# Kernel tuning notes

Hardware: AMD Instinct MI355X
Metric: run time of the kernel (lower is better)

Reference implementation:

```python
import jax, jax.numpy as jnp
import numpy as np

HIDDEN = 768
INTER = 1536
N_EXPERTS = 8
TOP_K = 2
AUX_COEF = 0.01


def setup_inputs() -> dict:
    key = jax.random.key(0)
    k0, k1, k2, k3, k4 = jax.random.split(key, 5)
    B, S = 2, 1024
    x = jax.random.normal(k0, (B, S, HIDDEN), dtype=jnp.float32)
    # nn.Linear weights (no bias); stored pre-transposed for einsum (in, out)
    router_w = jax.random.normal(k1, (HIDDEN, N_EXPERTS), dtype=jnp.float32) * 0.02
    w_gate = jax.random.normal(k2, (N_EXPERTS, HIDDEN, INTER), dtype=jnp.float32) * 0.02
    w_up = jax.random.normal(k3, (N_EXPERTS, HIDDEN, INTER), dtype=jnp.float32) * 0.02
    w_down = jax.random.normal(k4, (N_EXPERTS, INTER, HIDDEN), dtype=jnp.float32) * 0.02
    return {"x": x, "router_w": router_w, "w_gate": w_gate, "w_up": w_up, "w_down": w_down}


def reference(x, router_w, w_gate, w_up, w_down):
    B, S, H = x.shape
    xf = x.reshape(-1, H)                      # [T, H]
    T = xf.shape[0]

    router_logits = xf @ router_w              # [T, E]
    router_probs = jax.nn.softmax(router_logits.astype(jnp.float32), axis=-1)
    topk_probs, topk_idx = jax.lax.top_k(router_probs, TOP_K)   # [T, K]
    topk_probs = topk_probs / topk_probs.sum(axis=-1, keepdims=True)

    # dense combine weights: [T, E]; top_k indices are distinct per token so add == set
    comb = jnp.zeros((T, N_EXPERTS), jnp.float32).at[
        jnp.arange(T)[:, None], topk_idx
    ].add(topk_probs)

    # SwiGLU for all experts (dense faithful form of the per-expert gather loop)
    g = jnp.einsum("th,ehi->tei", xf, w_gate)  # [T, E, I]
    u = jnp.einsum("th,ehi->tei", xf, w_up)
    expert_out = jnp.einsum("tei,eih->teh", jax.nn.silu(g) * u, w_down)  # [T, E, H]
    out = jnp.einsum("teh,te->th", expert_out, comb.astype(expert_out.dtype))

    # load-balancing aux loss
    tokens_per_expert = jnp.zeros(N_EXPERTS, jnp.float32).at[topk_idx.reshape(-1)].add(1.0)
    tokens_per_expert = tokens_per_expert / (T * TOP_K)
    router_prob_per_expert = router_probs.mean(axis=0)
    aux_loss = N_EXPERTS * (tokens_per_expert * router_prob_per_expert).sum() * AUX_COEF

    return out.reshape(B, S, H), aux_loss
```

## Files before the change

kernel.cpp:

```cpp
#include <hip/hip_runtime.h>
#include <math.h>


typedef unsigned short u16;
typedef __attribute__((ext_vector_type(8))) short bhalf8;
typedef __attribute__((ext_vector_type(4))) float floatx4;

#define HD 768
#define ID 1536
#define NE 8
#define TT 2048
#define SLOTS 5120
#define MT 40
#define RBLK 512

__device__ __forceinline__ float b2f(u16 u) {
    union { unsigned int i; float f; } v; v.i = ((unsigned int)u) << 16; return v.f;
}
__device__ __forceinline__ u16 f2b(float f) {
    union { float f; unsigned int i; } v; v.f = f;
    unsigned int i = v.i;
    return (u16)((i + 0x7FFFu + ((i >> 16) & 1u)) >> 16);
}
__device__ __forceinline__ void glds16(const u16* g, u16* l) {
    __builtin_amdgcn_global_load_lds(
        (const __attribute__((address_space(1))) unsigned int*)g,
        (__attribute__((address_space(3))) unsigned int*)l, 16, 0, 0);
}

__global__ void init_k(const u16* __restrict__ x16, int* flag,
                       int* hdr, int* tokof, float* pslot) {
    int i = blockIdx.x * 256 + threadIdx.x;
    if (i < 40) hdr[i] = 0;
    if (i < SLOTS) { tokof[i] = -1; pslot[i] = 0.f; }
    if (blockIdx.x == 0 && threadIdx.x >= 64 && threadIdx.x < 128) {
        int lane = threadIdx.x - 64, c = 0;
#pragma unroll
        for (int j = 0; j < 4; ++j) {
            u16 w = x16[lane + 64 * j];
            int ex = (w >> 7) & 0xFF;
            c += (ex >= 118 && ex <= 135);
        }
#pragma unroll
        for (int off = 32; off > 0; off >>= 1) c += __shfl_xor(c, off);
        if (lane == 0) *flag = (c >= 200) ? 1 : 0;
    }
}

__global__ void router_k(const void* __restrict__ x, const void* __restrict__ rw,
                         const int* __restrict__ flag,
                         int* topki, float* topkp, float* blockpart) {
    __shared__ float sp[4][NE];
    int lane = threadIdx.x & 63, wave = threadIdx.x >> 6;
    int t = blockIdx.x * 4 + wave;
    int bf = *flag;
    const float* xf = (const float*)x + (size_t)t * HD;
    const u16*   xh = (const u16*)x + (size_t)t * HD;
    const float* rf = (const float*)rw;
    const u16*   rh = (const u16*)rw;
    float acc[NE];
#pragma unroll
    for (int e = 0; e < NE; ++e) acc[e] = 0.f;
    for (int j = 0; j < HD / 64; ++j) {
        int h = lane + 64 * j;
        float xv = bf ? b2f(xh[h]) : xf[h];
#pragma unroll
        for (int e = 0; e < NE; ++e)
            acc[e] += xv * (bf ? b2f(rh[h * NE + e]) : rf[h * NE + e]);
    }
#pragma unroll
    for (int e = 0; e < NE; ++e) {
        float v = acc[e];
#pragma unroll
        for (int off = 32; off > 0; off >>= 1) v += __shfl_xor(v, off);
        acc[e] = v;
    }
    if (lane == 0) {
        float m = acc[0];
        for (int e = 1; e < NE; ++e) m = fmaxf(m, acc[e]);
        float p[NE], s = 0.f;
        for (int e = 0; e < NE; ++e) { p[e] = expf(acc[e] - m); s += p[e]; }
        float inv = 1.f / s;
        for (int e = 0; e < NE; ++e) { p[e] *= inv; sp[wave][e] = p[e]; }
        int i1 = 0; float p1 = p[0];
        for (int e = 1; e < NE; ++e) if (p[e] > p1) { p1 = p[e]; i1 = e; }
        int i2 = -1; float p2 = -1.f;
        for (int e = 0; e < NE; ++e) if (e != i1 && p[e] > p2) { p2 = p[e]; i2 = e; }
        if (i2 < 0) { i2 = (i1 + 1) & 7; p2 = p[i2]; }
        float sn = 1.f / (p1 + p2);
        topki[2 * t] = i1;  topki[2 * t + 1] = i2;
        topkp[2 * t] = p1 * sn;  topkp[2 * t + 1] = p2 * sn;
    }
    __syncthreads();
    if (threadIdx.x < NE)
        blockpart[blockIdx.x * NE + threadIdx.x] =
            sp[0][threadIdx.x] + sp[1][threadIdx.x] +
            sp[2][threadIdx.x] + sp[3][threadIdx.x];
}

__global__ void prefix_k(const int* __restrict__ topki,
                         const float* __restrict__ blockpart, int* base,
                         int* total, int* cursor, void* out, const int* flag) {
    __shared__ int hist[NE];
    __shared__ float psum[NE];
    int tid = threadIdx.x;
    if (tid < NE) { hist[tid] = 0; psum[tid] = 0.f; }
    __syncthreads();
    for (int i = tid; i < TT * 2; i += 256) atomicAdd(&hist[topki[i] & 7], 1);
    for (int i = tid; i < RBLK * NE; i += 256) atomicAdd(&psum[i & 7], blockpart[i]);
    __syncthreads();
    if (tid == 0) {
        int cum = 0; float aux = 0.f;
        for (int e = 0; e < NE; ++e) {
            int c = hist[e];
            base[e] = cum; cum += (c + 127) & ~127;
            cursor[e] = 0;
            aux += ((float)c / (float)(TT * 2)) * (psum[e] / (float)TT);
        }
        *total = cum;
        float auxv = aux * (float)NE * 0.01f;
        if (*flag) ((u16*)out)[(size_t)TT * HD] = f2b(auxv);
        else       ((float*)out)[(size_t)TT * HD] = auxv;
    }
}

__global__ void scatter_k(const int* __restrict__ topki, const float* __restrict__ topkp,
                          const int* __restrict__ base, int* cursor,
                          int* tokof, float* pslot, int* slotmap) {
    __shared__ int lcnt[NE], lbase[NE];
    int tid = threadIdx.x;
    int t = blockIdx.x * 256 + tid;
    if (tid < NE) lcnt[tid] = 0;
    __syncthreads();
    int e0 = topki[2 * t] & 7, e1 = topki[2 * t + 1] & 7;
    float q0 = topkp[2 * t], q1 = topkp[2 * t + 1];
    int l0 = atomicAdd(&lcnt[e0], 1);
    int l1 = atomicAdd(&lcnt[e1], 1);
    __syncthreads();
    if (tid < NE) lbase[tid] = atomicAdd(&cursor[tid], lcnt[tid]);
    __syncthreads();
    int s0 = min(max(base[e0] + lbase[e0] + l0, 0), SLOTS - 1);
    int s1 = min(max(base[e1] + lbase[e1] + l1, 0), SLOTS - 1);
    tokof[s0] = t;  pslot[s0] = q0;  slotmap[2 * t] = s0;
    tokof[s1] = t;  pslot[s1] = q1;  slotmap[2 * t + 1] = s1;
}

__global__ void apack_k(const void* __restrict__ x, const int* __restrict__ flag,
                        const int* __restrict__ tokof, const int* __restrict__ total,
                        u16* __restrict__ apack) {
    int mt = blockIdx.y, kt = blockIdx.x;
    if (mt * 128 >= *total) return;
    int tid = threadIdx.x;
    int ml = tid >> 1, half = tid & 1;
    int tok = tokof[mt * 128 + ml];
    union { uint4 v[4]; u16 u[32]; } buf;
    if ((unsigned)tok < (unsigned)TT) {
        if (*flag) {
            const u16* s = (const u16*)x + (size_t)tok * HD + kt * 64 + half * 32;
#pragma unroll
            for (int c = 0; c < 4; ++c) buf.v[c] = *(const uint4*)&s[c * 8];
        } else {
            const float* s = (const float*)x + (size_t)tok * HD + kt * 64 + half * 32;
#pragma unroll
            for (int c = 0; c < 8; ++c) {
                float4 f = *(const float4*)&s[c * 4];
                buf.u[c * 4 + 0] = f2b(f.x); buf.u[c * 4 + 1] = f2b(f.y);
                buf.u[c * 4 + 2] = f2b(f.z); buf.u[c * 4 + 3] = f2b(f.w);
            }
        }
    } else {
#pragma unroll
        for (int c = 0; c < 4; ++c) buf.v[c] = make_uint4(0, 0, 0, 0);
    }
    u16* dst = apack + (((size_t)mt * 12 + kt) << 13) + ml * 64;
#pragma unroll
    for (int c = 0; c < 4; ++c) {
        int pc = (half * 4 + c) ^ (ml & 7);
        *(uint4*)(dst + pc * 8) = buf.v[c];
    }
}

__global__ void wpack_k(const void* __restrict__ srcA, const void* __restrict__ srcB,
                        u16* __restrict__ dstA, u16* __restrict__ dstB,
                        int K, int N, int ktiles, int ntiles,
                        const int* __restrict__ flag) {
    __shared__ u16 t[8192];
    int z = blockIdx.z;
    const void* src = (srcB != nullptr && z >= NE) ? srcB : srcA;
    u16* dst = (dstB != nullptr && z >= NE) ? dstB : dstA;
    int e = z & 7;
    int kt = blockIdx.x, nt = blockIdx.y;
    int tid = threadIdx.x;
    int kr = tid >> 2, ng = (tid & 3) * 32;
    size_t srow = ((size_t)e * K + (size_t)kt * 64 + kr) * N + (size_t)nt * 128 + ng;
    union { uint4 v[4]; u16 u[32]; } buf;
    if (*flag) {
        const u16* s = (const u16*)src + srow;
#pragma unroll
        for (int c = 0; c < 4; ++c) buf.v[c] = *(const uint4*)&s[c * 8];
    } else {
        const float* s = (const float*)src + srow;
#pragma unroll
        for (int c = 0; c < 8; ++c) {
            float4 f = *(const float4*)&s[c * 4];
            buf.u[c * 4 + 0] = f2b(f.x); buf.u[c * 4 + 1] = f2b(f.y);
            buf.u[c * 4 + 2] = f2b(f.z); buf.u[c * 4 + 3] = f2b(f.w);
        }
    }
#pragma unroll
    for (int jj = 0; jj < 32; ++jj) {
        int n = ng + jj;
        t[n * 64 + (((kr >> 3) ^ (n & 7)) << 3) + (kr & 7)] = buf.u[jj];
    }
    __syncthreads();
    u16* d = dst + ((((size_t)e * ntiles + nt) * ktiles + kt) << 13);
#pragma unroll
    for (int i = 0; i < 4; ++i) {
        int off = tid * 8 + i * 2048;
        *(uint4*)(d + off) = *(const uint4*)&t[off];
    }
}

__global__ __launch_bounds__(256, 2) void gemm1_k(
        const u16* __restrict__ apack, const u16* __restrict__ wgp,
        const u16* __restrict__ wup, const int* __restrict__ base,
        const int* __restrict__ total, u16* __restrict__ actp) {
    __shared__ u16 smem[24576];
    u16* As = smem; u16* Bg = smem + 8192; u16* Bu = smem + 16384;
    int mt = blockIdx.y;
    if (mt * 128 >= *total) return;
    int e = 7;
    while (e > 0 && mt * 128 < base[e]) --e;
    int nt = blockIdx.x;
    int tid = threadIdx.x, lane = tid & 63, wave = tid >> 6;
    int wm = (wave & 1) * 64, wn = (wave >> 1) * 64;
    int llo = lane & 15, lq = lane >> 4;
    const u16* atile = apack + (((size_t)mt * 12) << 13);
    const u16* gtile = wgp + ((((size_t)e * 12 + nt) * 12) << 13);
    const u16* utile = wup + ((((size_t)e * 12 + nt) * 12) << 13);
    floatx4 accG[4][4], accU[4][4];
#pragma unroll
    for (int i = 0; i < 4; ++i)
#pragma unroll
        for (int j = 0; j < 4; ++j) {
            accG[i][j] = floatx4{0.f, 0.f, 0.f, 0.f};
            accU[i][j] = floatx4{0.f, 0.f, 0.f, 0.f};
        }
    for (int kt = 0; kt < 12; ++kt) {
        const u16* ga = atile + (kt << 13);
        const u16* gg = gtile + (kt << 13);
        const u16* gu = utile + (kt << 13);
        __syncthreads();
#pragma unroll
        for (int i = 0; i < 4; ++i) {
            int off = tid * 8 + i * 2048;
            glds16(ga + off, As + off);
            glds16(gg + off, Bg + off);
            glds16(gu + off, Bu + off);
        }
        asm volatile("s_waitcnt vmcnt(0)" ::: "memory");
        __syncthreads();
#pragma unroll
        for (int kk = 0; kk < 2; ++kk) {
            int q = kk * 4 + lq;
            bhalf8 af[4], bg[4], bu[4];
#pragma unroll
            for (int i = 0; i < 4; ++i) {
                int m = wm + i * 16 + llo;
                af[i] = *(const bhalf8*)&As[m * 64 + ((q ^ (m & 7)) << 3)];
                int n = wn + i * 16 + llo;
                bg[i] = *(const bhalf8*)&Bg[n * 64 + ((q ^ (n & 7)) << 3)];
                bu[i] = *(const bhalf8*)&Bu[n * 64 + ((q ^ (n & 7)) << 3)];
            }
#pragma unroll
            for (int i = 0; i < 4; ++i)
#pragma unroll
                for (int j = 0; j < 4; ++j) {
                    accG[i][j] = __builtin_amdgcn_mfma_f32_16x16x32_bf16(af[i], bg[j], accG[i][j], 0, 0, 0);
                    accU[i][j] = __builtin_amdgcn_mfma_f32_16x16x32_bf16(af[i], bu[j], accU[i][j], 0, 0, 0);
                }
        }
    }
    __syncthreads();
    u16* Ah = smem;
    int q4 = lq * 4;
#pragma unroll
    for (int i = 0; i < 4; ++i)
#pragma unroll
        for (int j = 0; j < 4; ++j)
#pragma unroll
            for (int rr = 0; rr < 4; ++rr) {
                int m = wm + i * 16 + q4 + rr;
                int n = wn + j * 16 + llo;
                float g = accG[i][j][rr], u = accU[i][j][rr];
                Ah[m * 128 + n] = f2b((g / (1.f + expf(-g))) * u);
            }
    __syncthreads();
    u16* dst = actp + (((size_t)mt * 24 + nt * 2) << 13);
#pragma unroll
    for (int s = 0; s < 2; ++s)
#pragma unroll
        for (int i = 0; i < 4; ++i) {
            int off = tid * 8 + i * 2048;
            int m = off >> 6;
            int pc = (off >> 3) & 7;
            int q = pc ^ (m & 7);
            *(uint4*)(dst + ((size_t)s << 13) + off) =
                *(const uint4*)&Ah[m * 128 + s * 64 + q * 8];
        }
}

__global__ __launch_bounds__(256, 2) void gemm2_k(
        const u16* __restrict__ actp, const u16* __restrict__ wdp,
        const int* __restrict__ base, const int* __restrict__ total,
        const float* __restrict__ pslot, float* __restrict__ y) {
    __shared__ u16 smem[16384];
    u16* As = smem; u16* Bs = smem + 8192;
    int mt = blockIdx.y;
    if (mt * 128 >= *total) return;
    int e = 7;
    while (e > 0 && mt * 128 < base[e]) --e;
    int nt = blockIdx.x;
    int tid = threadIdx.x, lane = tid & 63, wave = tid >> 6;
    int wm = (wave & 1) * 64, wn = (wave >> 1) * 64;
    int llo = lane & 15, lq = lane >> 4;
    const u16* atile = actp + (((size_t)mt * 24) << 13);
    const u16* btile = wdp + ((((size_t)e * 6 + nt) * 24) << 13);
    floatx4 acc[4][4];
#pragma unroll
    for (int i = 0; i < 4; ++i)
#pragma unroll
        for (int j = 0; j < 4; ++j) acc[i][j] = floatx4{0.f, 0.f, 0.f, 0.f};
    for (int kt = 0; kt < 24; ++kt) {
        const u16* ga = atile + (kt << 13);
        const u16* gb = btile + (kt << 13);
        __syncthreads();
#pragma unroll
        for (int i = 0; i < 4; ++i) {
            int off = tid * 8 + i * 2048;
            glds16(ga + off, As + off);
            glds16(gb + off, Bs + off);
        }
        asm volatile("s_waitcnt vmcnt(0)" ::: "memory");
        __syncthreads();
#pragma unroll
        for (int kk = 0; kk < 2; ++kk) {
            int q = kk * 4 + lq;
            bhalf8 af[4], bf[4];
#pragma unroll
            for (int i = 0; i < 4; ++i) {
                int m = wm + i * 16 + llo;
                af[i] = *(const bhalf8*)&As[m * 64 + ((q ^ (m & 7)) << 3)];
                int n = wn + i * 16 + llo;
                bf[i] = *(const bhalf8*)&Bs[n * 64 + ((q ^ (n & 7)) << 3)];
            }
#pragma unroll
            for (int i = 0; i < 4; ++i)
#pragma unroll
                for (int j = 0; j < 4; ++j)
                    acc[i][j] = __builtin_amdgcn_mfma_f32_16x16x32_bf16(af[i], bf[j], acc[i][j], 0, 0, 0);
        }
    }
    int q4 = lq * 4;
#pragma unroll
    for (int i = 0; i < 4; ++i)
#pragma unroll
        for (int rr = 0; rr < 4; ++rr) {
            int m = mt * 128 + wm + i * 16 + q4 + rr;
            float p = pslot[m];
#pragma unroll
            for (int j = 0; j < 4; ++j) {
                int n = nt * 128 + wn + j * 16 + llo;
                y[(size_t)m * HD + n] = p * acc[i][j][rr];
            }
        }
}

__global__ void combine_k(const float* __restrict__ y, const int* __restrict__ slotmap,
                          void* __restrict__ out, const int* __restrict__ flag) {
    int g = blockIdx.x * 256 + threadIdx.x;
    int t = g / 192;
    int q = (g % 192) * 4;
    int s0 = min(max(slotmap[2 * t], 0), SLOTS - 1);
    int s1 = min(max(slotmap[2 * t + 1], 0), SLOTS - 1);
    float4 a = *(const float4*)&y[(size_t)s0 * HD + q];
    float4 b = *(const float4*)&y[(size_t)s1 * HD + q];
    float4 rv;
    rv.x = a.x + b.x; rv.y = a.y + b.y; rv.z = a.z + b.z; rv.w = a.w + b.w;
    if (*flag) {
        ushort4 o;
        o.x = f2b(rv.x); o.y = f2b(rv.y); o.z = f2b(rv.z); o.w = f2b(rv.w);
        *(ushort4*)((u16*)out + (size_t)t * HD + q) = o;
    } else {
        *(float4*)((float*)out + (size_t)t * HD + q) = rv;
    }
}

extern "C" void kernel_launch(void* const* d_in, const int* in_sizes, int n_in,
                              void* d_out, int out_size, void* d_ws, size_t ws_size,
                              hipStream_t stream) {
    const void* x  = d_in[0];
    const void* rw = d_in[1];
    const void* wg = d_in[2];
    const void* wu = d_in[3];
    const void* wd = d_in[4];
    char* ws = (char*)d_ws;

    int*   hdr     = (int*)(ws + 0);
    int*   cursor  = (int*)(ws + 32);
    int*   base    = (int*)(ws + 64);
    int*   total   = (int*)(ws + 96);
    int*   flag    = (int*)(ws + 224);
    int*   topki   = (int*)(ws + 256);
    float* topkp   = (float*)(ws + 16640);
    int*   tokof   = (int*)(ws + 33024);
    float* pslot   = (float*)(ws + 53504);
    int*   slotmap = (int*)(ws + 73984);
    float* blockpart = (float*)(ws + 90368);
    u16*   apack   = (u16*)(ws + 106752);
    u16*   actp    = (u16*)(ws + 7971072);
    u16*   wgp     = (u16*)(ws + 23699712);
    u16*   wup     = (u16*)(ws + 42574080);
    u16*   wdp     = (u16*)(ws + 61448448);
    float* ybuf    = (float*)(ws + 23699712);
    if (ws_size < 80322816u) return;

    init_k<<<20, 256, 0, stream>>>((const u16*)x, flag, hdr, tokof, pslot);
    router_k<<<RBLK, 256, 0, stream>>>(x, rw, flag, topki, topkp, blockpart);
    prefix_k<<<1, 256, 0, stream>>>(topki, blockpart, base, total, cursor, d_out, flag);
    scatter_k<<<TT / 256, 256, 0, stream>>>(topki, topkp, base, cursor,
                                            tokof, pslot, slotmap);
    apack_k<<<dim3(12, MT), 256, 0, stream>>>(x, flag, tokof, total, apack);
    wpack_k<<<dim3(12, 12, 16), 256, 0, stream>>>(wg, wu, wgp, wup,
                                                  HD, ID, 12, 12, flag);
    wpack_k<<<dim3(24, 6, 8), 256, 0, stream>>>(wd, nullptr, wdp, nullptr,
                                                ID, HD, 24, 6, flag);
    gemm1_k<<<dim3(12, MT), 256, 0, stream>>>(apack, wgp, wup, base, total, actp);
    gemm2_k<<<dim3(6, MT), 256, 0, stream>>>(actp, wdp, base, total, pslot, ybuf);
    combine_k<<<(TT * 192) / 256, 256, 0, stream>>>(ybuf, slotmap, d_out, flag);
}
```

Baseline: 266.8 us.

## Fuse init, router and weight packing into one launch; merge prefix and scatter

Ten kernel launches become six. Buffer init, the router, and packing of all three expert weight tensors now run as one kernel. Prefix sum, aux loss and scatter are merged into one 8-block kernel in which each block recomputes the histograms instead of using global atomic cursors. The bf16 flag is sniffed per block instead of stored in a global flag, so most kernels redo a small read of x. This cuts launch gaps and serial dependencies, at the cost of redundant histogram work and a larger, more heterogeneous setup kernel.

```diff
diff --git a/kernel.cpp b/kernel.cpp
--- a/kernel.cpp
+++ b/kernel.cpp
@@ -11,8 +11,6 @@
 #define NE 8
 #define TT 2048
 #define SLOTS 5120
-#define MT 40
-#define RBLK 512
 
 __device__ __forceinline__ float b2f(u16 u) {
     union { unsigned int i; float f; } v; v.i = ((unsigned int)u) << 16; return v.f;
@@ -27,135 +25,200 @@
         (const __attribute__((address_space(1))) unsigned int*)g,
         (__attribute__((address_space(3))) unsigned int*)l, 16, 0, 0);
 }
-
-__global__ void init_k(const u16* __restrict__ x16, int* flag,
-                       int* hdr, int* tokof, float* pslot) {
-    int i = blockIdx.x * 256 + threadIdx.x;
-    if (i < 40) hdr[i] = 0;
-    if (i < SLOTS) { tokof[i] = -1; pslot[i] = 0.f; }
-    if (blockIdx.x == 0 && threadIdx.x >= 64 && threadIdx.x < 128) {
-        int lane = threadIdx.x - 64, c = 0;
+__device__ __forceinline__ int sniff_bf(const u16* x16, int* sm, int tid) {
+    if (tid < 64) {
+        int c = 0;
 #pragma unroll
         for (int j = 0; j < 4; ++j) {
-            u16 w = x16[lane + 64 * j];
+            u16 w = x16[tid + 64 * j];
             int ex = (w >> 7) & 0xFF;
             c += (ex >= 118 && ex <= 135);
         }
 #pragma unroll
         for (int off = 32; off > 0; off >>= 1) c += __shfl_xor(c, off);
-        if (lane == 0) *flag = (c >= 200) ? 1 : 0;
-    }
-}
-
-__global__ void router_k(const void* __restrict__ x, const void* __restrict__ rw,
-                         const int* __restrict__ flag,
-                         int* topki, float* topkp, float* blockpart) {
-    __shared__ float sp[4][NE];
-    int lane = threadIdx.x & 63, wave = threadIdx.x >> 6;
-    int t = blockIdx.x * 4 + wave;
-    int bf = *flag;
-    const float* xf = (const float*)x + (size_t)t * HD;
-    const u16*   xh = (const u16*)x + (size_t)t * HD;
-    const float* rf = (const float*)rw;
-    const u16*   rh = (const u16*)rw;
-    float acc[NE];
-#pragma unroll
-    for (int e = 0; e < NE; ++e) acc[e] = 0.f;
-    for (int j = 0; j < HD / 64; ++j) {
-        int h = lane + 64 * j;
-        float xv = bf ? b2f(xh[h]) : xf[h];
-#pragma unroll
-        for (int e = 0; e < NE; ++e)
-            acc[e] += xv * (bf ? b2f(rh[h * NE + e]) : rf[h * NE + e]);
-    }
-#pragma unroll
-    for (int e = 0; e < NE; ++e) {
-        float v = acc[e];
-#pragma unroll
-        for (int off = 32; off > 0; off >>= 1) v += __shfl_xor(v, off);
-        acc[e] = v;
-    }
-    if (lane == 0) {
-        float m = acc[0];
-        for (int e = 1; e < NE; ++e) m = fmaxf(m, acc[e]);
-        float p[NE], s = 0.f;
-        for (int e = 0; e < NE; ++e) { p[e] = expf(acc[e] - m); s += p[e]; }
-        float inv = 1.f / s;
-        for (int e = 0; e < NE; ++e) { p[e] *= inv; sp[wave][e] = p[e]; }
-        int i1 = 0; float p1 = p[0];
-        for (int e = 1; e < NE; ++e) if (p[e] > p1) { p1 = p[e]; i1 = e; }
-        int i2 = -1; float p2 = -1.f;
-        for (int e = 0; e < NE; ++e) if (e != i1 && p[e] > p2) { p2 = p[e]; i2 = e; }
-        if (i2 < 0) { i2 = (i1 + 1) & 7; p2 = p[i2]; }
-        float sn = 1.f / (p1 + p2);
-        topki[2 * t] = i1;  topki[2 * t + 1] = i2;
-        topkp[2 * t] = p1 * sn;  topkp[2 * t + 1] = p2 * sn;
-    }
-    __syncthreads();
-    if (threadIdx.x < NE)
-        blockpart[blockIdx.x * NE + threadIdx.x] =
-            sp[0][threadIdx.x] + sp[1][threadIdx.x] +
-            sp[2][threadIdx.x] + sp[3][threadIdx.x];
-}
-
-__global__ void prefix_k(const int* __restrict__ topki,
-                         const float* __restrict__ blockpart, int* base,
-                         int* total, int* cursor, void* out, const int* flag) {
-    __shared__ int hist[NE];
+        if (tid == 0) *sm = (c >= 200) ? 1 : 0;
+    }
+    __syncthreads();
+    int bf = *sm;
+    __syncthreads();
+    return bf;
+}
+
+__global__ void setup_k(const void* __restrict__ x, const void* __restrict__ rw,
+                        const void* __restrict__ wg, const void* __restrict__ wu,
+                        const void* __restrict__ wd,
+                        int* __restrict__ tokof, float* __restrict__ pslot,
+                        int* __restrict__ topki, float* __restrict__ topkp,
+                        float* __restrict__ blockpart,
+                        u16* __restrict__ wgp, u16* __restrict__ wup,
+                        u16* __restrict__ wdp) {
+    __shared__ u16 smem[8192 + 64];
+    const int bid = blockIdx.x, tid = threadIdx.x;
+    const int lane = tid & 63, wave = tid >> 6;
+    int bf = sniff_bf((const u16*)x, (int*)(smem + 8192), tid);
+
+    {
+        int i = bid * 256 + tid;
+        if (i < SLOTS) { tokof[i] = -1; pslot[i] = 0.f; }
+    }
+
+    if (bid < 512) {
+        float* sp = (float*)(smem + 8192);
+        int t = bid * 4 + wave;
+        const float* xf = (const float*)x + (size_t)t * HD;
+        const u16*   xh = (const u16*)x + (size_t)t * HD;
+        const float* rf = (const float*)rw;
+        const u16*   rh = (const u16*)rw;
+        float acc[NE];
+#pragma unroll
+        for (int e = 0; e < NE; ++e) acc[e] = 0.f;
+        for (int j = 0; j < HD / 64; ++j) {
+            int h = lane + 64 * j;
+            float xv = bf ? b2f(xh[h]) : xf[h];
+#pragma unroll
+            for (int e = 0; e < NE; ++e)
+                acc[e] += xv * (bf ? b2f(rh[h * NE + e]) : rf[h * NE + e]);
+        }
+#pragma unroll
+        for (int e = 0; e < NE; ++e) {
+            float v = acc[e];
+#pragma unroll
+            for (int off = 32; off > 0; off >>= 1) v += __shfl_xor(v, off);
+            acc[e] = v;
+        }
+        if (lane == 0) {
+            float m = acc[0];
+            for (int e = 1; e < NE; ++e) m = fmaxf(m, acc[e]);
+            float p[NE], s = 0.f;
+            for (int e = 0; e < NE; ++e) { p[e] = expf(acc[e] - m); s += p[e]; }
+            float inv = 1.f / s;
+            for (int e = 0; e < NE; ++e) { p[e] *= inv; sp[wave * NE + e] = p[e]; }
+            int i1 = 0; float p1 = p[0];
+            for (int e = 1; e < NE; ++e) if (p[e] > p1) { p1 = p[e]; i1 = e; }
+            int i2 = -1; float p2 = -1.f;
+            for (int e = 0; e < NE; ++e) if (e != i1 && p[e] > p2) { p2 = p[e]; i2 = e; }
+            if (i2 < 0) { i2 = (i1 + 1) & 7; p2 = p[i2]; }
+            float sn = 1.f / (p1 + p2);
+            topki[2 * t] = i1;  topki[2 * t + 1] = i2;
+            topkp[2 * t] = p1 * sn;  topkp[2 * t + 1] = p2 * sn;
+        }
+        __syncthreads();
+        if (tid < NE)
+            blockpart[bid * NE + tid] =
+                sp[tid] + sp[NE + tid] + sp[2 * NE + tid] + sp[3 * NE + tid];
+        __syncthreads();
+    }
+
+    {
+        const void* src; u16* dst; int K, N, ktiles, ntiles, e, kt, nt;
+        if (bid < 2304) {
+            int z = bid / 144, rem = bid - z * 144;
+            nt = rem / 12; kt = rem - nt * 12;
+            e = z & 7;
+            src = (z < NE) ? wg : wu;
+            dst = (z < NE) ? wgp : wup;
+            K = HD; N = ID; ktiles = 12; ntiles = 12;
+        } else {
+            int T2 = bid - 2304;
+            e = T2 / 144; int rem = T2 - e * 144;
+            nt = rem / 24; kt = rem - nt * 24;
+            src = wd; dst = wdp; K = ID; N = HD; ktiles = 24; ntiles = 6;
+        }
+        int kr = tid >> 2, ng = (tid & 3) * 32;
+        size_t srow = ((size_t)e * K + (size_t)kt * 64 + kr) * N + (size_t)nt * 128 + ng;
+        union { uint4 v[4]; u16 u[32]; } buf;
+        if (bf) {
+            const u16* s = (const u16*)src + srow;
+#pragma unroll
+            for (int c = 0; c < 4; ++c) buf.v[c] = *(const uint4*)&s[c * 8];
+        } else {
+            const float* s = (const float*)src + srow;
+#pragma unroll
+            for (int c = 0; c < 8; ++c) {
+                float4 f = *(const float4*)&s[c * 4];
+                buf.u[c * 4 + 0] = f2b(f.x); buf.u[c * 4 + 1] = f2b(f.y);
+                buf.u[c * 4 + 2] = f2b(f.z); buf.u[c * 4 + 3] = f2b(f.w);
+            }
+        }
+#pragma unroll
+        for (int jj = 0; jj < 32; ++jj) {
+            int n = ng + jj;
+            smem[n * 64 + (((kr >> 3) ^ (n & 7)) << 3) + (kr & 7)] = buf.u[jj];
+        }
+        __syncthreads();
+        u16* d = dst + ((((size_t)e * ntiles + nt) * ktiles + kt) << 13);
+#pragma unroll
+        for (int i = 0; i < 4; ++i) {
+            int off = tid * 8 + i * 2048;
+            *(uint4*)(d + off) = *(const uint4*)&smem[off];
+        }
+    }
+}
+
+__global__ void sortscat_k(const void* __restrict__ x,
+                           const int* __restrict__ topki, const float* __restrict__ topkp,
+                           const float* __restrict__ blockpart,
+                           int* __restrict__ base, int* __restrict__ total,
+                           int* __restrict__ tokof, float* __restrict__ pslot,
+                           int* __restrict__ slotmap, void* __restrict__ out) {
+    __shared__ int tk[TT * 2];
+    __shared__ int histAll[NE], histPre[NE], lbase[NE], lcnt[NE];
     __shared__ float psum[NE];
-    int tid = threadIdx.x;
-    if (tid < NE) { hist[tid] = 0; psum[tid] = 0.f; }
-    __syncthreads();
-    for (int i = tid; i < TT * 2; i += 256) atomicAdd(&hist[topki[i] & 7], 1);
-    for (int i = tid; i < RBLK * NE; i += 256) atomicAdd(&psum[i & 7], blockpart[i]);
+    __shared__ int sm1;
+    const int bid = blockIdx.x, tid = threadIdx.x;
+    int bf = sniff_bf((const u16*)x, &sm1, tid);
+    if (tid < NE) { histAll[tid] = 0; histPre[tid] = 0; lcnt[tid] = 0; psum[tid] = 0.f; }
+    __syncthreads();
+    int pre_end = 2 * bid * 256;
+    for (int i = tid; i < TT * 2; i += 256) {
+        int e = topki[i] & 7;
+        tk[i] = e;
+        atomicAdd(&histAll[e], 1);
+        if (i < pre_end) atomicAdd(&histPre[e], 1);
+    }
+    if (bid == 0)
+        for (int i = tid; i < 512 * NE; i += 256) atomicAdd(&psum[i & 7], blockpart[i]);
     __syncthreads();
     if (tid == 0) {
         int cum = 0; float aux = 0.f;
         for (int e = 0; e < NE; ++e) {
-            int c = hist[e];
-            base[e] = cum; cum += (c + 127) & ~127;
-            cursor[e] = 0;
-            aux += ((float)c / (float)(TT * 2)) * (psum[e] / (float)TT);
-        }
-        *total = cum;
-        float auxv = aux * (float)NE * 0.01f;
-        if (*flag) ((u16*)out)[(size_t)TT * HD] = f2b(auxv);
-        else       ((float*)out)[(size_t)TT * HD] = auxv;
-    }
-}
-
-__global__ void scatter_k(const int* __restrict__ topki, const float* __restrict__ topkp,
-                          const int* __restrict__ base, int* cursor,
-                          int* tokof, float* pslot, int* slotmap) {
-    __shared__ int lcnt[NE], lbase[NE];
-    int tid = threadIdx.x;
-    int t = blockIdx.x * 256 + tid;
-    if (tid < NE) lcnt[tid] = 0;
-    __syncthreads();
-    int e0 = topki[2 * t] & 7, e1 = topki[2 * t + 1] & 7;
+            lbase[e] = cum;
+            cum += (histAll[e] + 127) & ~127;
+            aux += ((float)histAll[e] / (float)(TT * 2)) * (psum[e] / (float)TT);
+        }
+        if (bid == 0) {
+            for (int e = 0; e < NE; ++e) base[e] = lbase[e];
+            *total = cum;
+            float auxv = aux * (float)NE * 0.01f;
+            if (bf) ((u16*)out)[(size_t)TT * HD] = f2b(auxv);
+            else    ((float*)out)[(size_t)TT * HD] = auxv;
+        }
+    }
+    __syncthreads();
+    int t = bid * 256 + tid;
+    int e0 = tk[2 * t], e1 = tk[2 * t + 1];
     float q0 = topkp[2 * t], q1 = topkp[2 * t + 1];
     int l0 = atomicAdd(&lcnt[e0], 1);
     int l1 = atomicAdd(&lcnt[e1], 1);
-    __syncthreads();
-    if (tid < NE) lbase[tid] = atomicAdd(&cursor[tid], lcnt[tid]);
-    __syncthreads();
-    int s0 = min(max(base[e0] + lbase[e0] + l0, 0), SLOTS - 1);
-    int s1 = min(max(base[e1] + lbase[e1] + l1, 0), SLOTS - 1);
+    int s0 = min(max(lbase[e0] + histPre[e0] + l0, 0), SLOTS - 1);
+    int s1 = min(max(lbase[e1] + histPre[e1] + l1, 0), SLOTS - 1);
     tokof[s0] = t;  pslot[s0] = q0;  slotmap[2 * t] = s0;
     tokof[s1] = t;  pslot[s1] = q1;  slotmap[2 * t + 1] = s1;
 }
 
-__global__ void apack_k(const void* __restrict__ x, const int* __restrict__ flag,
+__global__ void apack_k(const void* __restrict__ x,
                         const int* __restrict__ tokof, const int* __restrict__ total,
                         u16* __restrict__ apack) {
+    __shared__ int sm1;
+    int tid = threadIdx.x;
+    int bf = sniff_bf((const u16*)x, &sm1, tid);
     int mt = blockIdx.y, kt = blockIdx.x;
     if (mt * 128 >= *total) return;
-    int tid = threadIdx.x;
     int ml = tid >> 1, half = tid & 1;
     int tok = tokof[mt * 128 + ml];
     union { uint4 v[4]; u16 u[32]; } buf;
     if ((unsigned)tok < (unsigned)TT) {
-        if (*flag) {
+        if (bf) {
             const u16* s = (const u16*)x + (size_t)tok * HD + kt * 64 + half * 32;
 #pragma unroll
             for (int c = 0; c < 4; ++c) buf.v[c] = *(const uint4*)&s[c * 8];
@@ -177,47 +240,6 @@
     for (int c = 0; c < 4; ++c) {
         int pc = (half * 4 + c) ^ (ml & 7);
         *(uint4*)(dst + pc * 8) = buf.v[c];
-    }
-}
-
-__global__ void wpack_k(const void* __restrict__ srcA, const void* __restrict__ srcB,
-                        u16* __restrict__ dstA, u16* __restrict__ dstB,
-                        int K, int N, int ktiles, int ntiles,
-                        const int* __restrict__ flag) {
-    __shared__ u16 t[8192];
-    int z = blockIdx.z;
-    const void* src = (srcB != nullptr && z >= NE) ? srcB : srcA;
-    u16* dst = (dstB != nullptr && z >= NE) ? dstB : dstA;
-    int e = z & 7;
-    int kt = blockIdx.x, nt = blockIdx.y;
-    int tid = threadIdx.x;
-    int kr = tid >> 2, ng = (tid & 3) * 32;
-    size_t srow = ((size_t)e * K + (size_t)kt * 64 + kr) * N + (size_t)nt * 128 + ng;
-    union { uint4 v[4]; u16 u[32]; } buf;
-    if (*flag) {
-        const u16* s = (const u16*)src + srow;
-#pragma unroll
-        for (int c = 0; c < 4; ++c) buf.v[c] = *(const uint4*)&s[c * 8];
-    } else {
-        const float* s = (const float*)src + srow;
-#pragma unroll
-        for (int c = 0; c < 8; ++c) {
-            float4 f = *(const float4*)&s[c * 4];
-            buf.u[c * 4 + 0] = f2b(f.x); buf.u[c * 4 + 1] = f2b(f.y);
-            buf.u[c * 4 + 2] = f2b(f.z); buf.u[c * 4 + 3] = f2b(f.w);
-        }
-    }
-#pragma unroll
-    for (int jj = 0; jj < 32; ++jj) {
-        int n = ng + jj;
-        t[n * 64 + (((kr >> 3) ^ (n & 7)) << 3) + (kr & 7)] = buf.u[jj];
-    }
-    __syncthreads();
-    u16* d = dst + ((((size_t)e * ntiles + nt) * ktiles + kt) << 13);
-#pragma unroll
-    for (int i = 0; i < 4; ++i) {
-        int off = tid * 8 + i * 2048;
-        *(uint4*)(d + off) = *(const uint4*)&t[off];
     }
 }
 
@@ -346,19 +368,19 @@
 #pragma unroll
         for (int kk = 0; kk < 2; ++kk) {
             int q = kk * 4 + lq;
-            bhalf8 af[4], bf[4];
+            bhalf8 af[4], bfr[4];
 #pragma unroll
             for (int i = 0; i < 4; ++i) {
                 int m = wm + i * 16 + llo;
                 af[i] = *(const bhalf8*)&As[m * 64 + ((q ^ (m & 7)) << 3)];
                 int n = wn + i * 16 + llo;
-                bf[i] = *(const bhalf8*)&Bs[n * 64 + ((q ^ (n & 7)) << 3)];
+                bfr[i] = *(const bhalf8*)&Bs[n * 64 + ((q ^ (n & 7)) << 3)];
             }
 #pragma unroll
             for (int i = 0; i < 4; ++i)
 #pragma unroll
                 for (int j = 0; j < 4; ++j)
-                    acc[i][j] = __builtin_amdgcn_mfma_f32_16x16x32_bf16(af[i], bf[j], acc[i][j], 0, 0, 0);
+                    acc[i][j] = __builtin_amdgcn_mfma_f32_16x16x32_bf16(af[i], bfr[j], acc[i][j], 0, 0, 0);
         }
     }
     int q4 = lq * 4;
@@ -376,18 +398,21 @@
         }
 }
 
-__global__ void combine_k(const float* __restrict__ y, const int* __restrict__ slotmap,
-                          void* __restrict__ out, const int* __restrict__ flag) {
-    int g = blockIdx.x * 256 + threadIdx.x;
+__global__ void combine_k(const void* __restrict__ x, const float* __restrict__ y,
+                          const int* __restrict__ slotmap, void* __restrict__ out) {
+    __shared__ int sm1;
+    int tid = threadIdx.x;
+    int bf = sniff_bf((const u16*)x, &sm1, tid);
+    int g = blockIdx.x * 256 + tid;
     int t = g / 192;
-    int q = (g % 192) * 4;
+    int q = (g - t * 192) * 4;
     int s0 = min(max(slotmap[2 * t], 0), SLOTS - 1);
     int s1 = min(max(slotmap[2 * t + 1], 0), SLOTS - 1);
     float4 a = *(const float4*)&y[(size_t)s0 * HD + q];
     float4 b = *(const float4*)&y[(size_t)s1 * HD + q];
     float4 rv;
     rv.x = a.x + b.x; rv.y = a.y + b.y; rv.z = a.z + b.z; rv.w = a.w + b.w;
-    if (*flag) {
+    if (bf) {
         ushort4 o;
         o.x = f2b(rv.x); o.y = f2b(rv.y); o.z = f2b(rv.z); o.w = f2b(rv.w);
         *(ushort4*)((u16*)out + (size_t)t * HD + q) = o;
@@ -399,6 +424,7 @@
 extern "C" void kernel_launch(void* const* d_in, const int* in_sizes, int n_in,
                               void* d_out, int out_size, void* d_ws, size_t ws_size,
                               hipStream_t stream) {
+    if (ws_size < 80322816u) return;
     const void* x  = d_in[0];
     const void* rw = d_in[1];
     const void* wg = d_in[2];
@@ -406,15 +432,12 @@
     const void* wd = d_in[4];
     char* ws = (char*)d_ws;
 
-    int*   hdr     = (int*)(ws + 0);
-    int*   cursor  = (int*)(ws + 32);
-    int*   base    = (int*)(ws + 64);
-    int*   total   = (int*)(ws + 96);
-    int*   flag    = (int*)(ws + 224);
+    int*   basep   = (int*)(ws + 64);
+    int*   totalp  = (int*)(ws + 96);
     int*   topki   = (int*)(ws + 256);
     float* topkp   = (float*)(ws + 16640);
     int*   tokof   = (int*)(ws + 33024);
-    float* pslot   = (float*)(ws + 53504);
+    float* pslotp  = (float*)(ws + 53504);
     int*   slotmap = (int*)(ws + 73984);
     float* blockpart = (float*)(ws + 90368);
     u16*   apack   = (u16*)(ws + 106752);
@@ -423,19 +446,13 @@
     u16*   wup     = (u16*)(ws + 42574080);
     u16*   wdp     = (u16*)(ws + 61448448);
     float* ybuf    = (float*)(ws + 23699712);
-    if (ws_size < 80322816u) return;
-
-    init_k<<<20, 256, 0, stream>>>((const u16*)x, flag, hdr, tokof, pslot);
-    router_k<<<RBLK, 256, 0, stream>>>(x, rw, flag, topki, topkp, blockpart);
-    prefix_k<<<1, 256, 0, stream>>>(topki, blockpart, base, total, cursor, d_out, flag);
-    scatter_k<<<TT / 256, 256, 0, stream>>>(topki, topkp, base, cursor,
-                                            tokof, pslot, slotmap);
-    apack_k<<<dim3(12, MT), 256, 0, stream>>>(x, flag, tokof, total, apack);
-    wpack_k<<<dim3(12, 12, 16), 256, 0, stream>>>(wg, wu, wgp, wup,
-                                                  HD, ID, 12, 12, flag);
-    wpack_k<<<dim3(24, 6, 8), 256, 0, stream>>>(wd, nullptr, wdp, nullptr,
-                                                ID, HD, 24, 6, flag);
-    gemm1_k<<<dim3(12, MT), 256, 0, stream>>>(apack, wgp, wup, base, total, actp);
-    gemm2_k<<<dim3(6, MT), 256, 0, stream>>>(actp, wdp, base, total, pslot, ybuf);
-    combine_k<<<(TT * 192) / 256, 256, 0, stream>>>(ybuf, slotmap, d_out, flag);
-}
+
+    setup_k<<<3456, 256, 0, stream>>>(x, rw, wg, wu, wd, tokof, pslotp,
+                                      topki, topkp, blockpart, wgp, wup, wdp);
+    sortscat_k<<<8, 256, 0, stream>>>(x, topki, topkp, blockpart, basep, totalp,
+                                      tokof, pslotp, slotmap, d_out);
+    apack_k<<<dim3(12, 40), 256, 0, stream>>>(x, tokof, totalp, apack);
+    gemm1_k<<<dim3(12, 40), 256, 0, stream>>>(apack, wgp, wup, basep, totalp, actp);
+    gemm2_k<<<dim3(6, 40), 256, 0, stream>>>(actp, wdp, basep, totalp, pslotp, ybuf);
+    combine_k<<<1536, 256, 0, stream>>>(x, ybuf, slotmap, d_out);
+}
```

New measurement: 246.4 us. 1.08x faster.
